# Optimization experiments

Hardware: AMD Instinct MI355X
Metric: run time of the kernel (lower is better)

The kernel has to match this reference:

```python
import jax, jax.numpy as jnp
import numpy as np

TEMPERATURE = 8.0  # sqrt(d_k=64)


def setup_inputs() -> dict:
    key = jax.random.key(0)
    ks = jax.random.split(key, 7)
    B, Lq, Lk, H, DK, DV, R, R2 = 4, 1024, 1024, 8, 64, 64, 32, 16
    return {
        "q":    jax.random.normal(ks[0], (B, Lq, H, DK), jnp.float32),
        "W_A":  jax.random.normal(ks[1], (H, DK, R),  jnp.float32) * 0.1,
        "W_B":  jax.random.normal(ks[2], (H, R, R2),  jnp.float32) * 0.1,
        "W_At": jax.random.normal(ks[3], (H, R, DK),  jnp.float32) * 0.1,
        "W_Bt": jax.random.normal(ks[4], (H, R2, R),  jnp.float32) * 0.1,
        "qt":   jax.random.normal(ks[5], (B, H, DK, Lk), jnp.float32),
        "v":    jax.random.normal(ks[6], (B, H, Lk, DV), jnp.float32),
        "d_k":  64,
        "mask": jnp.ones((B, 1, Lq, Lk), dtype=bool),
    }


def reference(q, W_A, W_B, W_At, W_Bt, qt, v, d_k, mask):
    # Low-rank projection chain: q -> A -> B -> Bt -> At  (per head b)
    IA      = jnp.einsum('kabc,bcd->kabd', q, W_A)        # [B,Lq,H,R]
    IAB     = jnp.einsum('kabj,bji->kabi', IA, W_B)       # [B,Lq,H,R2]
    IABBt   = jnp.einsum('kabi,bim->kabm', IAB, W_Bt)     # [B,Lq,H,R]
    IABBtAt = jnp.einsum('kabm,bmj->kabj', IABBt, W_At)   # [B,Lq,H,DK]
    # Bilinear score against transposed keys qt: [B,H,DK,Lk]
    attn = jnp.einsum('kabj,kbjm->kbam', IABBtAt, qt) / TEMPERATURE  # [B,H,Lq,Lk]
    attn = jnp.where(mask, attn, -1e9)
    attn = jax.nn.softmax(attn, axis=-1)
    # dropout p=0 (inference/reference) -> identity
    output = jnp.matmul(attn, v)  # [B,H,Lq,DV]
    return output, attn
```

## Files before the change

kernel.cpp:

```cpp
#include <hip/hip_runtime.h>

typedef short short8 __attribute__((ext_vector_type(8)));
typedef float f32x4 __attribute__((ext_vector_type(4)));

__device__ inline unsigned short f2bf(float f) {
    unsigned u = __builtin_bit_cast(unsigned, f);
    u += 0x7fff + ((u >> 16) & 1);
    return (unsigned short)(u >> 16);
}
__device__ inline short8 as_short8(uint4 v) { return __builtin_bit_cast(short8, v); }

__global__ __launch_bounds__(256) void repack_kernel(const float* __restrict__ qt,
                                                     const float* __restrict__ v,
                                                     uint4* __restrict__ qtp,
                                                     uint4* __restrict__ vp) {
    const int tid = threadIdx.x;
    int g = blockIdx.x * 256 + tid;
    int lane = g & 63;
    const float* src;
    uint4* dst;
    size_t jstride;
    if (g < 262144) {
        int kc = (g >> 6) & 1;
        int nt = (g >> 7) & 63;
        int bh = g >> 13;
        int k = kc * 32 + (lane >> 4) * 8;
        int n = nt * 16 + (lane & 15);
        src = qt + ((size_t)bh * 64 + k) * 1024 + n;
        jstride = 1024;
        dst = qtp + g;
    } else {
        int g2 = g - 262144;
        int kc = (g2 >> 6) & 31;
        int nt = (g2 >> 11) & 3;
        int bh = g2 >> 13;
        int k = kc * 32 + (lane >> 4) * 8;
        int n = nt * 16 + (lane & 15);
        src = v + ((size_t)bh * 1024 + k) * 64 + n;
        jstride = 64;
        dst = vp + g2;
    }
    unsigned short e[8];
#pragma unroll
    for (int j = 0; j < 8; ++j) e[j] = f2bf(src[jstride * j]);
    uint4 o;
    o.x = e[0] | ((unsigned)e[1] << 16);
    o.y = e[2] | ((unsigned)e[3] << 16);
    o.z = e[4] | ((unsigned)e[5] << 16);
    o.w = e[6] | ((unsigned)e[7] << 16);
    *dst = o;
}

__global__ __launch_bounds__(256, 4) void attn_kernel(
    const float* __restrict__ q,
    const float* __restrict__ WA,
    const float* __restrict__ WB,
    const float* __restrict__ WBt,
    const float* __restrict__ WAt,
    const uint4* __restrict__ qtp,
    const uint4* __restrict__ vp,
    float* __restrict__ outp,
    float* __restrict__ attnp) {
    constexpr int PST = 1032;
    __shared__ __align__(16) union {
        struct {
            float qrow[16 * 64];
            float WAl[64 * 32];
            float WBl[32 * 16];
            float WBtl[16 * 32];
            float WAtl[32 * 64];
            float IA[16 * 32];
            float IAB[16 * 16];
            float IBT[16 * 32];
        } s;
        unsigned short Pbuf[16 * PST];
    } u;
    __shared__ __align__(16) unsigned short Qpl[16 * 72];
    __shared__ float redsum[4][16];

    const int tid = threadIdx.x;
    const int w = tid >> 6, lane = tid & 63;
    const int quad = lane >> 4, l16 = lane & 15;
    const int bh = blockIdx.x & 31;
    const int mblk = blockIdx.x >> 5;
    const int b = bh >> 3, h = bh & 7;
    const int rb = mblk * 16;
    const int rowbase = bh * 1024 + rb;

#pragma unroll
    for (int i = 0; i < 4; ++i) {
        int e = i * 256 + tid;
        int row = e >> 6, k = e & 63;
        u.s.qrow[e] = q[((size_t)(b * 1024 + rb + row) * 8 + h) * 64 + k];
    }
#pragma unroll
    for (int i = 0; i < 8; ++i) u.s.WAl[i * 256 + tid] = WA[h * 2048 + i * 256 + tid];
#pragma unroll
    for (int i = 0; i < 2; ++i) u.s.WBl[i * 256 + tid] = WB[h * 512 + i * 256 + tid];
#pragma unroll
    for (int i = 0; i < 2; ++i) u.s.WBtl[i * 256 + tid] = WBt[h * 512 + i * 256 + tid];
#pragma unroll
    for (int i = 0; i < 8; ++i) u.s.WAtl[i * 256 + tid] = WAt[h * 2048 + i * 256 + tid];
    __syncthreads();
#pragma unroll
    for (int i = 0; i < 2; ++i) {
        int e = i * 256 + tid;
        int row = e >> 5, c = e & 31;
        float s = 0.f;
#pragma unroll
        for (int j = 0; j < 64; ++j) s += u.s.qrow[row * 64 + j] * u.s.WAl[j * 32 + c];
        u.s.IA[e] = s;
    }
    __syncthreads();
    {
        int row = tid >> 4, c = tid & 15;
        float s = 0.f;
#pragma unroll
        for (int j = 0; j < 32; ++j) s += u.s.IA[row * 32 + j] * u.s.WBl[j * 16 + c];
        u.s.IAB[tid] = s;
    }
    __syncthreads();
#pragma unroll
    for (int i = 0; i < 2; ++i) {
        int e = i * 256 + tid;
        int row = e >> 5, c = e & 31;
        float s = 0.f;
#pragma unroll
        for (int j = 0; j < 16; ++j) s += u.s.IAB[row * 16 + j] * u.s.WBtl[j * 32 + c];
        u.s.IBT[e] = s;
    }
    __syncthreads();
    constexpr float QSCALE = 0.125f * 1.4426950408889634f;
#pragma unroll
    for (int i = 0; i < 4; ++i) {
        int e = i * 256 + tid;
        int row = e >> 6, k = e & 63;
        float s = 0.f;
#pragma unroll
        for (int j = 0; j < 32; ++j) s += u.s.IBT[row * 32 + j] * u.s.WAtl[j * 64 + k];
        Qpl[row * 72 + k] = f2bf(s * QSCALE);
    }
    __syncthreads();

    const unsigned short* qpl = &Qpl[l16 * 72 + quad * 8];
    short8 a0 = as_short8(*(const uint4*)(qpl));
    short8 a1 = as_short8(*(const uint4*)(qpl + 32));

    f32x4 acc[16];
    const uint4* qtb = qtp + (size_t)bh * 8192 + lane;
#pragma unroll
    for (int t = 0; t < 16; ++t) {
        int nt = w * 16 + t;
        uint4 b0 = qtb[(nt * 2 + 0) * 64];
        uint4 b1 = qtb[(nt * 2 + 1) * 64];
        f32x4 z = {0.f, 0.f, 0.f, 0.f};
        z = __builtin_amdgcn_mfma_f32_16x16x32_bf16(as_short8(b0), a0, z, 0, 0, 0);
        acc[t] = __builtin_amdgcn_mfma_f32_16x16x32_bf16(as_short8(b1), a1, z, 0, 0, 0);
    }

    constexpr float SHIFT2 = 8.0f * 1.4426950408889634f;
    float sum = 0.f;
#pragma unroll
    for (int t = 0; t < 16; ++t) {
#pragma unroll
        for (int r = 0; r < 4; ++r) {
            float p = exp2f(acc[t][r] - SHIFT2);
            acc[t][r] = p;
            sum += p;
        }
    }
    sum += __shfl_xor(sum, 16, 64);
    sum += __shfl_xor(sum, 32, 64);
    if (lane < 16) redsum[w][l16] = sum;
    __syncthreads();
    const float inv = 1.0f / (redsum[0][l16] + redsum[1][l16] +
                              redsum[2][l16] + redsum[3][l16]);

    const uint4* vb = vp + (size_t)bh * 8192 + (size_t)w * 32 * 64 + lane;
    uint4 pf0 = vb[0 * 64];
    uint4 pf1 = vb[1 * 64];
    uint4 pf2 = vb[2 * 64];
    uint4 pf3 = vb[3 * 64];

    float* abase = attnp + ((size_t)(rowbase + l16)) * 1024 + w * 256 + quad * 4;
    unsigned short* pbase = &u.Pbuf[l16 * PST + w * 256 + quad * 4];
#pragma unroll
    for (int t = 0; t < 16; ++t) {
        f32x4 p;
        p[0] = acc[t][0] * inv;
        p[1] = acc[t][1] * inv;
        p[2] = acc[t][2] * inv;
        p[3] = acc[t][3] * inv;
        __builtin_nontemporal_store(p, reinterpret_cast<f32x4*>(abase + t * 16));
        uint2 d;
        d.x = f2bf(p[0]) | ((unsigned)f2bf(p[1]) << 16);
        d.y = f2bf(p[2]) | ((unsigned)f2bf(p[3]) << 16);
        *reinterpret_cast<uint2*>(pbase + t * 16) = d;
    }
    __syncthreads();

    f32x4 o = {0.f, 0.f, 0.f, 0.f};
    const unsigned short* prow = &u.Pbuf[l16 * PST + quad * 8];
#pragma unroll
    for (int kc = 0; kc < 32; ++kc) {
        short8 a = as_short8(*(const uint4*)(prow + kc * 32));
        uint4 bfrag = (kc == 0) ? pf0 : (kc == 1) ? pf1 : (kc == 2) ? pf2 : (kc == 3) ? pf3
                                      : vb[kc * 64];
        o = __builtin_amdgcn_mfma_f32_16x16x32_bf16(as_short8(bfrag), a, o, 0, 0, 0);
    }
    __builtin_nontemporal_store(
        o, reinterpret_cast<f32x4*>(outp + ((size_t)(rowbase + l16)) * 64 + w * 16 + quad * 4));
}

extern "C" void kernel_launch(void* const* d_in, const int* in_sizes, int n_in,
                              void* d_out, int out_size, void* d_ws, size_t ws_size,
                              hipStream_t stream) {
    (void)in_sizes; (void)n_in; (void)out_size; (void)ws_size;
    const float* q   = (const float*)d_in[0];
    const float* WA  = (const float*)d_in[1];
    const float* WB  = (const float*)d_in[2];
    const float* WAt = (const float*)d_in[3];
    const float* WBt = (const float*)d_in[4];
    const float* qt  = (const float*)d_in[5];
    const float* v   = (const float*)d_in[6];

    float* outp  = (float*)d_out;
    float* attnp = outp + (size_t)4 * 8 * 1024 * 64;

    char* ws = (char*)d_ws;
    uint4* qtp = (uint4*)ws;
    uint4* vp  = (uint4*)(ws + 4194304);

    hipLaunchKernelGGL(repack_kernel, dim3(2048), dim3(256), 0, stream, qt, v, qtp, vp);
    hipLaunchKernelGGL(attn_kernel, dim3(2048), dim3(256), 0, stream,
                       q, WA, WB, WBt, WAt, qtp, vp, outp, attnp);
}
```

Baseline: 221.1 us.

## Precompute combined low-rank weight per head and defer softmax normalization past PV

The four per-head projection weights are multiplied into one 64x64 matrix by extra blocks in the repack kernel. The attention kernel then does a single q·Wc product instead of four chained small matmuls with their barriers. Unnormalized probabilities are written to LDS as bf16 before the row-sum reduction, so one barrier is dropped. The PV output is scaled by the inverse sum afterwards, which moves the PV MFMA ahead of the large attn stores. The cost is a few extra FLOPs per row and an extra workspace round trip for Wc, plus small rounding differences from the reassociation.

```diff
diff --git a/kernel.cpp b/kernel.cpp
--- a/kernel.cpp
+++ b/kernel.cpp
@@ -12,9 +12,62 @@
 
 __global__ __launch_bounds__(256) void repack_kernel(const float* __restrict__ qt,
                                                      const float* __restrict__ v,
+                                                     const float* __restrict__ WA,
+                                                     const float* __restrict__ WB,
+                                                     const float* __restrict__ WBt,
+                                                     const float* __restrict__ WAt,
                                                      uint4* __restrict__ qtp,
-                                                     uint4* __restrict__ vp) {
+                                                     uint4* __restrict__ vp,
+                                                     float* __restrict__ Wc) {
     const int tid = threadIdx.x;
+    if (blockIdx.x >= 2048) {
+        __shared__ float WAl[64 * 32];
+        __shared__ float WBl[32 * 16];
+        __shared__ float WBtl[16 * 32];
+        __shared__ float WAtl[32 * 64];
+        __shared__ float T1[64 * 16];
+        __shared__ float T2[64 * 32];
+        int h = blockIdx.x - 2048;
+#pragma unroll
+        for (int i = 0; i < 8; ++i) WAl[i * 256 + tid] = WA[h * 2048 + i * 256 + tid];
+#pragma unroll
+        for (int i = 0; i < 2; ++i) WBl[i * 256 + tid] = WB[h * 512 + i * 256 + tid];
+#pragma unroll
+        for (int i = 0; i < 2; ++i) WBtl[i * 256 + tid] = WBt[h * 512 + i * 256 + tid];
+#pragma unroll
+        for (int i = 0; i < 8; ++i) WAtl[i * 256 + tid] = WAt[h * 2048 + i * 256 + tid];
+        __syncthreads();
+#pragma unroll
+        for (int i = 0; i < 4; ++i) {
+            int e = i * 256 + tid;
+            int r = e >> 4, c = e & 15;
+            float s = 0.f;
+#pragma unroll
+            for (int j = 0; j < 32; ++j) s += WAl[r * 32 + j] * WBl[j * 16 + c];
+            T1[e] = s;
+        }
+        __syncthreads();
+#pragma unroll
+        for (int i = 0; i < 8; ++i) {
+            int e = i * 256 + tid;
+            int r = e >> 5, c = e & 31;
+            float s = 0.f;
+#pragma unroll
+            for (int j = 0; j < 16; ++j) s += T1[r * 16 + j] * WBtl[j * 32 + c];
+            T2[e] = s;
+        }
+        __syncthreads();
+#pragma unroll
+        for (int i = 0; i < 16; ++i) {
+            int e = i * 256 + tid;
+            int r = e >> 6, c = e & 63;
+            float s = 0.f;
+#pragma unroll
+            for (int j = 0; j < 32; ++j) s += T2[r * 32 + j] * WAtl[j * 64 + c];
+            Wc[h * 4096 + e] = s;
+        }
+        return;
+    }
     int g = blockIdx.x * 256 + tid;
     int lane = g & 63;
     const float* src;
@@ -53,10 +106,7 @@
 
 __global__ __launch_bounds__(256, 4) void attn_kernel(
     const float* __restrict__ q,
-    const float* __restrict__ WA,
-    const float* __restrict__ WB,
-    const float* __restrict__ WBt,
-    const float* __restrict__ WAt,
+    const float* __restrict__ Wc,
     const uint4* __restrict__ qtp,
     const uint4* __restrict__ vp,
     float* __restrict__ outp,
@@ -65,13 +115,7 @@
     __shared__ __align__(16) union {
         struct {
             float qrow[16 * 64];
-            float WAl[64 * 32];
-            float WBl[32 * 16];
-            float WBtl[16 * 32];
-            float WAtl[32 * 64];
-            float IA[16 * 32];
-            float IAB[16 * 16];
-            float IBT[16 * 32];
+            float Wl[64 * 64];
         } s;
         unsigned short Pbuf[16 * PST];
     } u;
@@ -94,41 +138,7 @@
         u.s.qrow[e] = q[((size_t)(b * 1024 + rb + row) * 8 + h) * 64 + k];
     }
 #pragma unroll
-    for (int i = 0; i < 8; ++i) u.s.WAl[i * 256 + tid] = WA[h * 2048 + i * 256 + tid];
-#pragma unroll
-    for (int i = 0; i < 2; ++i) u.s.WBl[i * 256 + tid] = WB[h * 512 + i * 256 + tid];
-#pragma unroll
-    for (int i = 0; i < 2; ++i) u.s.WBtl[i * 256 + tid] = WBt[h * 512 + i * 256 + tid];
-#pragma unroll
-    for (int i = 0; i < 8; ++i) u.s.WAtl[i * 256 + tid] = WAt[h * 2048 + i * 256 + tid];
-    __syncthreads();
-#pragma unroll
-    for (int i = 0; i < 2; ++i) {
-        int e = i * 256 + tid;
-        int row = e >> 5, c = e & 31;
-        float s = 0.f;
-#pragma unroll
-        for (int j = 0; j < 64; ++j) s += u.s.qrow[row * 64 + j] * u.s.WAl[j * 32 + c];
-        u.s.IA[e] = s;
-    }
-    __syncthreads();
-    {
-        int row = tid >> 4, c = tid & 15;
-        float s = 0.f;
-#pragma unroll
-        for (int j = 0; j < 32; ++j) s += u.s.IA[row * 32 + j] * u.s.WBl[j * 16 + c];
-        u.s.IAB[tid] = s;
-    }
-    __syncthreads();
-#pragma unroll
-    for (int i = 0; i < 2; ++i) {
-        int e = i * 256 + tid;
-        int row = e >> 5, c = e & 31;
-        float s = 0.f;
-#pragma unroll
-        for (int j = 0; j < 16; ++j) s += u.s.IAB[row * 16 + j] * u.s.WBtl[j * 32 + c];
-        u.s.IBT[e] = s;
-    }
+    for (int i = 0; i < 16; ++i) u.s.Wl[i * 256 + tid] = Wc[h * 4096 + i * 256 + tid];
     __syncthreads();
     constexpr float QSCALE = 0.125f * 1.4426950408889634f;
 #pragma unroll
@@ -137,7 +147,7 @@
         int row = e >> 6, k = e & 63;
         float s = 0.f;
 #pragma unroll
-        for (int j = 0; j < 32; ++j) s += u.s.IBT[row * 32 + j] * u.s.WAtl[j * 64 + k];
+        for (int j = 0; j < 64; ++j) s += u.s.qrow[row * 64 + j] * u.s.Wl[j * 64 + k];
         Qpl[row * 72 + k] = f2bf(s * QSCALE);
     }
     __syncthreads();
@@ -169,12 +179,18 @@
             sum += p;
         }
     }
+
+    unsigned short* pbase = &u.Pbuf[l16 * PST + w * 256 + quad * 4];
+#pragma unroll
+    for (int t = 0; t < 16; ++t) {
+        uint2 d;
+        d.x = f2bf(acc[t][0]) | ((unsigned)f2bf(acc[t][1]) << 16);
+        d.y = f2bf(acc[t][2]) | ((unsigned)f2bf(acc[t][3]) << 16);
+        *reinterpret_cast<uint2*>(pbase + t * 16) = d;
+    }
     sum += __shfl_xor(sum, 16, 64);
     sum += __shfl_xor(sum, 32, 64);
     if (lane < 16) redsum[w][l16] = sum;
-    __syncthreads();
-    const float inv = 1.0f / (redsum[0][l16] + redsum[1][l16] +
-                              redsum[2][l16] + redsum[3][l16]);
 
     const uint4* vb = vp + (size_t)bh * 8192 + (size_t)w * 32 * 64 + lane;
     uint4 pf0 = vb[0 * 64];
@@ -182,8 +198,24 @@
     uint4 pf2 = vb[2 * 64];
     uint4 pf3 = vb[3 * 64];
 
+    __syncthreads();
+    const float inv = 1.0f / (redsum[0][l16] + redsum[1][l16] +
+                              redsum[2][l16] + redsum[3][l16]);
+
+    f32x4 o = {0.f, 0.f, 0.f, 0.f};
+    const unsigned short* prow = &u.Pbuf[l16 * PST + quad * 8];
+#pragma unroll
+    for (int kc = 0; kc < 32; ++kc) {
+        short8 a = as_short8(*(const uint4*)(prow + kc * 32));
+        uint4 bfrag = (kc == 0) ? pf0 : (kc == 1) ? pf1 : (kc == 2) ? pf2 : (kc == 3) ? pf3
+                                      : vb[kc * 64];
+        o = __builtin_amdgcn_mfma_f32_16x16x32_bf16(as_short8(bfrag), a, o, 0, 0, 0);
+    }
+    o[0] *= inv; o[1] *= inv; o[2] *= inv; o[3] *= inv;
+    __builtin_nontemporal_store(
+        o, reinterpret_cast<f32x4*>(outp + ((size_t)(rowbase + l16)) * 64 + w * 16 + quad * 4));
+
     float* abase = attnp + ((size_t)(rowbase + l16)) * 1024 + w * 256 + quad * 4;
-    unsigned short* pbase = &u.Pbuf[l16 * PST + w * 256 + quad * 4];
 #pragma unroll
     for (int t = 0; t < 16; ++t) {
         f32x4 p;
@@ -192,24 +224,7 @@
         p[2] = acc[t][2] * inv;
         p[3] = acc[t][3] * inv;
         __builtin_nontemporal_store(p, reinterpret_cast<f32x4*>(abase + t * 16));
-        uint2 d;
-        d.x = f2bf(p[0]) | ((unsigned)f2bf(p[1]) << 16);
-        d.y = f2bf(p[2]) | ((unsigned)f2bf(p[3]) << 16);
-        *reinterpret_cast<uint2*>(pbase + t * 16) = d;
-    }
-    __syncthreads();
-
-    f32x4 o = {0.f, 0.f, 0.f, 0.f};
-    const unsigned short* prow = &u.Pbuf[l16 * PST + quad * 8];
-#pragma unroll
-    for (int kc = 0; kc < 32; ++kc) {
-        short8 a = as_short8(*(const uint4*)(prow + kc * 32));
-        uint4 bfrag = (kc == 0) ? pf0 : (kc == 1) ? pf1 : (kc == 2) ? pf2 : (kc == 3) ? pf3
-                                      : vb[kc * 64];
-        o = __builtin_amdgcn_mfma_f32_16x16x32_bf16(as_short8(bfrag), a, o, 0, 0, 0);
-    }
-    __builtin_nontemporal_store(
-        o, reinterpret_cast<f32x4*>(outp + ((size_t)(rowbase + l16)) * 64 + w * 16 + quad * 4));
+    }
 }
 
 extern "C" void kernel_launch(void* const* d_in, const int* in_sizes, int n_in,
@@ -230,8 +245,10 @@
     char* ws = (char*)d_ws;
     uint4* qtp = (uint4*)ws;
     uint4* vp  = (uint4*)(ws + 4194304);
-
-    hipLaunchKernelGGL(repack_kernel, dim3(2048), dim3(256), 0, stream, qt, v, qtp, vp);
+    float* Wc  = (float*)(ws + 2 * 4194304);
+
+    hipLaunchKernelGGL(repack_kernel, dim3(2056), dim3(256), 0, stream,
+                       qt, v, WA, WB, WBt, WAt, qtp, vp, Wc);
     hipLaunchKernelGGL(attn_kernel, dim3(2048), dim3(256), 0, stream,
-                       q, WA, WB, WBt, WAt, qtp, vp, outp, attnp);
-}
+                       q, Wc, qtp, vp, outp, attnp);
+}
```

After: 255.5 us. 15.6% more time.
